# Kernel tuning notes

Measured on AMD Instinct MI355X. Metric: run time of the kernel, lower is better.

## Reference

```python
import jax, jax.numpy as jnp
import numpy as np

B, T, C = 2, 2048, 1024
N_HEAD, N_GROUP = 16, 4
N_KV = N_HEAD // N_GROUP          # 4
HEAD_DIM = C // N_HEAD            # 64
ROPE_BASE = 10000.0
INIT_STD = 0.02


def setup_inputs() -> dict:
    key = jax.random.key(0)
    ks = jax.random.split(key, 5)
    kvC = N_KV * HEAD_DIM
    return {
        "x": jax.random.normal(ks[0], (B, T, C), jnp.float32),
        "w_q": jax.random.normal(ks[1], (C, C), jnp.float32) * INIT_STD,
        "b_q": jnp.zeros((C,), jnp.float32),
        "w_k": jax.random.normal(ks[2], (C, kvC), jnp.float32) * INIT_STD,
        "b_k": jnp.zeros((kvC,), jnp.float32),
        "w_v": jax.random.normal(ks[3], (C, kvC), jnp.float32) * INIT_STD,
        "b_v": jnp.zeros((kvC,), jnp.float32),
        "w_o": jax.random.normal(ks[4], (C, C), jnp.float32) * INIT_STD,
        "b_o": jnp.zeros((C,), jnp.float32),
    }


def reference(x, w_q, b_q, w_k, b_k, w_v, b_v, w_o, b_o):
    Bx, Tx, Cx = x.shape
    # projections (torch Linear math with weights stored as [in, out])
    q = (x @ w_q + b_q).reshape(Bx, Tx, N_HEAD, HEAD_DIM).transpose(0, 2, 1, 3)  # [B,H,T,hd]
    k = (x @ w_k + b_k).reshape(Bx, Tx, N_KV, HEAD_DIM).transpose(0, 2, 1, 3)    # [B,KV,T,hd]
    v = (x @ w_v + b_v).reshape(Bx, Tx, N_KV, HEAD_DIM).transpose(0, 2, 1, 3)

    # RoPE with INTERLEAVED pair convention: pairs are (dim 2i, dim 2i+1)
    inv_freq = 1.0 / (ROPE_BASE ** (jnp.arange(0, HEAD_DIM, 2, dtype=jnp.float32) / HEAD_DIM))
    freqs = jnp.arange(Tx, dtype=jnp.float32)[:, None] * inv_freq[None, :]       # [T, hd/2]
    cos, sin = jnp.cos(freqs), jnp.sin(freqs)

    def rope(t):
        tp = t.reshape(*t.shape[:-1], HEAD_DIM // 2, 2)
        e, o = tp[..., 0], tp[..., 1]          # even/odd lanes, [B,h,T,hd/2]
        er = e * cos - o * sin
        orr = e * sin + o * cos
        return jnp.stack([er, orr], axis=-1).reshape(t.shape)

    q, k = rope(q), rope(k)

    # GQA: duplicate each KV head n_group times (consecutively, like repeat_interleave)
    k = jnp.repeat(k, N_GROUP, axis=1)   # [B,H,T,hd]
    v = jnp.repeat(v, N_GROUP, axis=1)

    attn = jnp.einsum('bhqd,bhkd->bhqk', q, k) / np.sqrt(HEAD_DIM).astype(np.float32)
    causal = jnp.tril(jnp.ones((Tx, Tx), bool))
    attn = jnp.where(causal, attn, -jnp.inf)
    attn = jax.nn.softmax(attn, axis=-1)

    out = jnp.einsum('bhqk,bhkd->bhqd', attn, v)            # [B,H,T,hd]
    out = out.transpose(0, 2, 1, 3).reshape(Bx, Tx, Cx)
    return out @ w_o + b_o
```

## Files before the change

kernel.cpp:

```cpp
#include <hip/hip_runtime.h>
#include <hip/hip_bf16.h>

typedef __hip_bfloat16 bf16;
typedef __attribute__((ext_vector_type(8))) short short8_t;
typedef __attribute__((ext_vector_type(4))) short short4_t;
typedef __attribute__((ext_vector_type(4))) float f32x4;

#define B_SZ   2
#define T_SEQ  2048
#define C_DIM  1024
#define NH     16
#define NKV    4
#define HD     64
#define QKVW   1536
#define MTOK   (B_SZ * T_SEQ)

#define LOG2_BASE_OVER_32 0.4152410118609203f
#define Q_SCALE 0.1803368801111204f

__device__ __forceinline__ short f2bs(float f) {
    unsigned u = __float_as_uint(f);
    u += 0x7FFFu + ((u >> 16) & 1u);
    return (short)(u >> 16);
}
__device__ __forceinline__ short f2bs_trunc(float f) {
    return (short)(__float_as_uint(f) >> 16);
}
__device__ __forceinline__ float bs2f(short s) {
    unsigned u = ((unsigned)(unsigned short)s) << 16;
    return __uint_as_float(u);
}
__device__ __forceinline__ float dpp_xor1(float x) {
    return __int_as_float(
        __builtin_amdgcn_update_dpp(0, __float_as_int(x), 0xB1, 0xF, 0xF, true));
}

__device__ __forceinline__ void transpose_tile(
    const float* __restrict__ W, short* __restrict__ Wt,
    int K, int N, int n0, int k0, int tid)
{
    __shared__ float tile[32][33];
    int tx = tid & 31, ty = tid >> 5;
    #pragma unroll
    for (int i = 0; i < 4; ++i)
        tile[ty + 8 * i][tx] = W[(size_t)(k0 + ty + 8 * i) * N + n0 + tx];
    __syncthreads();
    #pragma unroll
    for (int i = 0; i < 4; ++i)
        Wt[(size_t)(n0 + ty + 8 * i) * K + k0 + tx] = f2bs(tile[tx][ty + 8 * i]);
}

__global__ __launch_bounds__(256) void prep_kernel(
    const float* __restrict__ x,
    const float* __restrict__ w_q, const float* __restrict__ w_k,
    const float* __restrict__ w_v, const float* __restrict__ w_o,
    const float* __restrict__ b_q, const float* __restrict__ b_k,
    const float* __restrict__ b_v,
    short* __restrict__ Xb, short* __restrict__ Wqkv, short* __restrict__ Wto,
    float* __restrict__ Bqkv, float2* __restrict__ Tab)
{
    int blk = blockIdx.x, tid = threadIdx.x;
    if (blk < 4096) {
        int i = blk * 1024 + tid * 4;
        float4 v = *(const float4*)(x + i);
        short4_t o;
        o[0] = f2bs(v.x); o[1] = f2bs(v.y); o[2] = f2bs(v.z); o[3] = f2bs(v.w);
        *(short4_t*)(Xb + i) = o;
    } else if (blk < 5120) {
        int l = blk - 4096;
        transpose_tile(w_q, Wqkv, C_DIM, C_DIM, (l & 31) * 32, (l >> 5) * 32, tid);
    } else if (blk < 5376) {
        int l = blk - 5120;
        transpose_tile(w_k, Wqkv + (size_t)1024 * C_DIM, C_DIM, 256,
                       (l & 7) * 32, (l >> 3) * 32, tid);
    } else if (blk < 5632) {
        int l = blk - 5376;
        transpose_tile(w_v, Wqkv + (size_t)1280 * C_DIM, C_DIM, 256,
                       (l & 7) * 32, (l >> 3) * 32, tid);
    } else if (blk < 6656) {
        int l = blk - 5632;
        transpose_tile(w_o, Wto, C_DIM, C_DIM, (l & 31) * 32, (l >> 5) * 32, tid);
    } else if (blk < 6662) {
        int i = (blk - 6656) * 256 + tid;
        float v;
        if (i < 1024)      v = b_q[i];
        else if (i < 1280) v = b_k[i - 1024];
        else               v = b_v[i - 1280];
        Bqkv[i] = v;
    } else {
        int idx = (blk - 6662) * 256 + tid;
        int t = idx >> 5, i = idx & 31;
        float ang = (float)t * exp2f(-(float)i * LOG2_BASE_OVER_32);
        Tab[idx] = make_float2(cosf(ang), sinf(ang));
    }
}

__global__ __launch_bounds__(256) void gemm_qkv(
    const short* __restrict__ A, const short* __restrict__ Bt,
    const float* __restrict__ bias, const float2* __restrict__ Tab,
    short* __restrict__ QKVb, short* __restrict__ Vt)
{
    __shared__ __align__(16) short smem[20480];
    typedef short lds_tile_t[128][40];
    lds_tile_t* sA = (lds_tile_t*)smem;
    lds_tile_t* sB = (lds_tile_t*)(smem + 10240);

    const int K = C_DIM, N = QKVW;
    int m0 = blockIdx.y * 128;
    int n0 = blockIdx.x * 128;
    int tid  = threadIdx.x;
    int w    = tid >> 6, lane = tid & 63;
    int quad = lane >> 4, l16 = lane & 15;
    int wm = w & 1, wn = w >> 1;

    f32x4 acc[4][4] = {};

    short8_t ra[2], rb[2];
    #pragma unroll
    for (int it = 0; it < 2; ++it) {
        int slot = tid + 256 * it, row = slot >> 2, g = (slot & 3) * 8;
        ra[it] = *(const short8_t*)(A  + (size_t)(m0 + row) * K + g);
        rb[it] = *(const short8_t*)(Bt + (size_t)(n0 + row) * K + g);
    }

    int buf = 0;
    for (int k0 = 0; k0 < K; k0 += 32, buf ^= 1) {
        #pragma unroll
        for (int it = 0; it < 2; ++it) {
            int slot = tid + 256 * it, row = slot >> 2, g = (slot & 3) * 8;
            *(short8_t*)&sA[buf][row][g] = ra[it];
            *(short8_t*)&sB[buf][row][g] = rb[it];
        }
        if (k0 + 32 < K) {
            #pragma unroll
            for (int it = 0; it < 2; ++it) {
                int slot = tid + 256 * it, row = slot >> 2, g = (slot & 3) * 8;
                ra[it] = *(const short8_t*)(A  + (size_t)(m0 + row) * K + k0 + 32 + g);
                rb[it] = *(const short8_t*)(Bt + (size_t)(n0 + row) * K + k0 + 32 + g);
            }
        }
        __syncthreads();

        short8_t af[4], bfr[4];
        #pragma unroll
        for (int mt = 0; mt < 4; ++mt)
            af[mt] = *(const short8_t*)&sA[buf][wm * 64 + mt * 16 + l16][quad * 8];
        #pragma unroll
        for (int nt = 0; nt < 4; ++nt)
            bfr[nt] = *(const short8_t*)&sB[buf][wn * 64 + nt * 16 + l16][quad * 8];
        #pragma unroll
        for (int mt = 0; mt < 4; ++mt)
            #pragma unroll
            for (int nt = 0; nt < 4; ++nt)
                acc[mt][nt] = __builtin_amdgcn_mfma_f32_16x16x32_bf16(
                    af[mt], bfr[nt], acc[mt][nt], 0, 0, 0);
    }

    if (n0 < 1280) {
        float scale = (n0 < 1024) ? Q_SCALE : 1.0f;
        float sgn   = (l16 & 1) ? 1.0f : -1.0f;
        #pragma unroll
        for (int nt = 0; nt < 4; ++nt) {
            int col = n0 + wn * 64 + nt * 16 + l16;
            int ip  = (col & 63) >> 1;
            float bv = bias[col];
            #pragma unroll
            for (int mt = 0; mt < 4; ++mt) {
                #pragma unroll
                for (int r = 0; r < 4; ++r) {
                    int row = m0 + wm * 64 + mt * 16 + quad * 4 + r;
                    float v = acc[mt][nt][r] + bv;
                    float po = dpp_xor1(v);
                    float2 cs = Tab[(row & (T_SEQ - 1)) * 32 + ip];
                    float res = (v * cs.x + sgn * po * cs.y) * scale;
                    QKVb[(size_t)row * QKVW + col] = f2bs(res);
                }
            }
        }
    } else {
        __syncthreads();
        short (*sT)[136] = (short(*)[136])smem;
        #pragma unroll
        for (int nt = 0; nt < 4; ++nt) {
            int col_l = wn * 64 + nt * 16 + l16;
            float bv = bias[n0 + col_l];
            #pragma unroll
            for (int mt = 0; mt < 4; ++mt)
                #pragma unroll
                for (int r = 0; r < 4; ++r)
                    sT[col_l][wm * 64 + mt * 16 + quad * 4 + r] =
                        f2bs(acc[mt][nt][r] + bv);
        }
        __syncthreads();
        int d0 = n0 - 1280;
        #pragma unroll
        for (int it = 0; it < 8; ++it) {
            int slot = tid + 256 * it;
            int dl = slot >> 4, seg = (slot & 15) * 8;
            *(short8_t*)(Vt + (size_t)(d0 + dl) * MTOK + m0 + seg) =
                *(const short8_t*)&sT[dl][seg];
        }
    }
}

__global__ __launch_bounds__(256) void gemm_mfma_o(
    const short* __restrict__ A, const short* __restrict__ Bt,
    const float* __restrict__ bias, float* __restrict__ C,
    int M, int N, int K)
{
    __shared__ __align__(16) short sA[2][128][40];
    __shared__ __align__(16) short sB[2][128][40];

    int m0 = blockIdx.y * 128;
    int n0 = blockIdx.x * 128;
    int tid  = threadIdx.x;
    int w    = tid >> 6, lane = tid & 63;
    int quad = lane >> 4, l16 = lane & 15;
    int wm = w & 1, wn = w >> 1;

    f32x4 acc[4][4] = {};

    short8_t ra[2], rb[2];
    #pragma unroll
    for (int it = 0; it < 2; ++it) {
        int slot = tid + 256 * it, row = slot >> 2, g = (slot & 3) * 8;
        ra[it] = *(const short8_t*)(A  + (size_t)(m0 + row) * K + g);
        rb[it] = *(const short8_t*)(Bt + (size_t)(n0 + row) * K + g);
    }

    int buf = 0;
    for (int k0 = 0; k0 < K; k0 += 32, buf ^= 1) {
        #pragma unroll
        for (int it = 0; it < 2; ++it) {
            int slot = tid + 256 * it, row = slot >> 2, g = (slot & 3) * 8;
            *(short8_t*)&sA[buf][row][g] = ra[it];
            *(short8_t*)&sB[buf][row][g] = rb[it];
        }
        if (k0 + 32 < K) {
            #pragma unroll
            for (int it = 0; it < 2; ++it) {
                int slot = tid + 256 * it, row = slot >> 2, g = (slot & 3) * 8;
                ra[it] = *(const short8_t*)(A  + (size_t)(m0 + row) * K + k0 + 32 + g);
                rb[it] = *(const short8_t*)(Bt + (size_t)(n0 + row) * K + k0 + 32 + g);
            }
        }
        __syncthreads();

        short8_t af[4], bfr[4];
        #pragma unroll
        for (int mt = 0; mt < 4; ++mt)
            af[mt] = *(const short8_t*)&sA[buf][wm * 64 + mt * 16 + l16][quad * 8];
        #pragma unroll
        for (int nt = 0; nt < 4; ++nt)
            bfr[nt] = *(const short8_t*)&sB[buf][wn * 64 + nt * 16 + l16][quad * 8];
        #pragma unroll
        for (int mt = 0; mt < 4; ++mt)
            #pragma unroll
            for (int nt = 0; nt < 4; ++nt)
                acc[mt][nt] = __builtin_amdgcn_mfma_f32_16x16x32_bf16(
                    af[mt], bfr[nt], acc[mt][nt], 0, 0, 0);
    }

    #pragma unroll
    for (int mt = 0; mt < 4; ++mt) {
        #pragma unroll
        for (int nt = 0; nt < 4; ++nt) {
            int col = n0 + wn * 64 + nt * 16 + l16;
            float bv = bias[col];
            #pragma unroll
            for (int r = 0; r < 4; ++r) {
                int row = m0 + wm * 64 + mt * 16 + quad * 4 + r;
                C[(size_t)row * N + col] = acc[mt][nt][r] + bv;
            }
        }
    }
}

__global__ __launch_bounds__(256) void attn_mfma7(
    const short* __restrict__ QKV, const short* __restrict__ Vt,
    short* __restrict__ O)
{
    __shared__ __align__(16) short sK [128][72];
    __shared__ __align__(16) short sVt[64][136];
    __shared__ __align__(16) short sP [4][16][136];

    const int tid  = threadIdx.x;
    const int w    = tid >> 6;
    const int lane = tid & 63;
    const int quad = lane >> 4;
    const int l16  = lane & 15;

    int blk = blockIdx.x;
    int grp = blk & 7;
    int tq  = 127 - (blk >> 3);
    int kvh = grp & 3;
    int b   = grp >> 2;
    int h   = kvh * 4 + w;
    int ct  = (tq * 16 + 15) >> 7;
    int tg  = tq * 16 + l16;

    const short* qptr = QKV + ((size_t)(b * T_SEQ + tq * 16 + l16)) * QKVW + h * HD;
    short8_t qf0 = *(const short8_t*)(qptr + quad * 8);
    short8_t qf1 = *(const short8_t*)(qptr + quad * 8 + 32);

    const short* kbase  = QKV + (size_t)b * T_SEQ * QKVW + 1024 + kvh * HD;
    const short* vtbase = Vt + (size_t)(kvh * HD) * MTOK + b * T_SEQ;

    float m_l = -INFINITY, l_l = 0.f;
    f32x4 oacc[4];
    #pragma unroll
    for (int dt = 0; dt < 4; ++dt) oacc[dt] = (f32x4){0.f, 0.f, 0.f, 0.f};

    short8_t kr[4], vr[4];
    #pragma unroll
    for (int it = 0; it < 4; ++it) {
        int slot = tid + 256 * it;
        kr[it] = *(const short8_t*)(kbase + (size_t)(slot >> 3) * QKVW + (slot & 7) * 8);
        vr[it] = *(const short8_t*)(vtbase + (size_t)(slot >> 4) * MTOK + (slot & 15) * 8);
    }

    for (int c = 0; c <= ct; ++c) {
        __syncthreads();
        #pragma unroll
        for (int it = 0; it < 4; ++it) {
            int slot = tid + 256 * it;
            *(short8_t*)&sK [slot >> 3][(slot & 7) * 8]  = kr[it];
            *(short8_t*)&sVt[slot >> 4][(slot & 15) * 8] = vr[it];
        }
        __syncthreads();
        if (c < ct) {
            int jn = (c + 1) * 128;
            #pragma unroll
            for (int it = 0; it < 4; ++it) {
                int slot = tid + 256 * it;
                kr[it] = *(const short8_t*)(kbase + (size_t)(jn + (slot >> 3)) * QKVW + (slot & 7) * 8);
                vr[it] = *(const short8_t*)(vtbase + (size_t)(slot >> 4) * MTOK + jn + (slot & 15) * 8);
            }
        }

        f32x4 sacc[8];
        #pragma unroll
        for (int kt = 0; kt < 8; ++kt) {
            f32x4 z = {0.f, 0.f, 0.f, 0.f};
            short8_t kf0 = *(const short8_t*)&sK[l16 + 16 * kt][quad * 8];
            short8_t kf1 = *(const short8_t*)&sK[l16 + 16 * kt][quad * 8 + 32];
            z = __builtin_amdgcn_mfma_f32_16x16x32_bf16(kf0, qf0, z, 0, 0, 0);
            z = __builtin_amdgcn_mfma_f32_16x16x32_bf16(kf1, qf1, z, 0, 0, 0);
            sacc[kt] = z;
        }

        if (c == ct) {
            int j0 = c * 128;
            #pragma unroll
            for (int kt = 0; kt < 8; ++kt)
                #pragma unroll
                for (int r = 0; r < 4; ++r)
                    if (j0 + 16 * kt + quad * 4 + r > tg) sacc[kt][r] = -INFINITY;
        }

        float vmax = sacc[0][0];
        #pragma unroll
        for (int kt = 0; kt < 8; ++kt)
            #pragma unroll
            for (int r = 0; r < 4; ++r) vmax = fmaxf(vmax, sacc[kt][r]);
        vmax = fmaxf(vmax, __shfl_xor(vmax, 16));
        vmax = fmaxf(vmax, __shfl_xor(vmax, 32));
        float mnew = fmaxf(m_l, vmax);
        float al = exp2f(m_l - mnew);
        m_l = mnew;

        float psum = 0.f;
        #pragma unroll
        for (int kt = 0; kt < 8; ++kt) {
            short4_t pk;
            #pragma unroll
            for (int r = 0; r < 4; ++r) {
                float p = exp2f(sacc[kt][r] - mnew);
                psum += p;
                pk[r] = f2bs_trunc(p);
            }
            *(short4_t*)&sP[w][l16][16 * kt + 4 * quad] = pk;
        }
        psum += __shfl_xor(psum, 16);
        psum += __shfl_xor(psum, 32);
        l_l = l_l * al + psum;

        if (__any(al < 1.f)) {
            #pragma unroll
            for (int r = 0; r < 4; ++r) {
                float alr = __shfl(al, quad * 4 + r);
                #pragma unroll
                for (int dt = 0; dt < 4; ++dt) oacc[dt][r] *= alr;
            }
        }

        short8_t pf[4];
        #pragma unroll
        for (int g = 0; g < 4; ++g)
            pf[g] = *(const short8_t*)&sP[w][l16][32 * g + quad * 8];
        #pragma unroll
        for (int dt = 0; dt < 4; ++dt) {
            #pragma unroll
            for (int g = 0; g < 4; ++g) {
                short8_t vf = *(const short8_t*)&sVt[16 * dt + l16][32 * g + quad * 8];
                oacc[dt] = __builtin_amdgcn_mfma_f32_16x16x32_bf16(pf[g], vf, oacc[dt], 0, 0, 0);
            }
        }
    }

    #pragma unroll
    for (int r = 0; r < 4; ++r) {
        int m = quad * 4 + r;
        float lr = __shfl(l_l, quad * 4 + r);
        float inv = __builtin_amdgcn_rcpf(lr);
        #pragma unroll
        for (int dt = 0; dt < 4; ++dt)
            O[((size_t)b * T_SEQ + tq * 16 + m) * C_DIM + h * HD + 16 * dt + l16] =
                f2bs(oacc[dt][r] * inv);
    }
}

extern "C" void kernel_launch(void* const* d_in, const int* in_sizes, int n_in,
                              void* d_out, int out_size, void* d_ws, size_t ws_size,
                              hipStream_t stream)
{
    const float* x   = (const float*)d_in[0];
    const float* w_q = (const float*)d_in[1];
    const float* b_q = (const float*)d_in[2];
    const float* w_k = (const float*)d_in[3];
    const float* b_k = (const float*)d_in[4];
    const float* w_v = (const float*)d_in[5];
    const float* b_v = (const float*)d_in[6];
    const float* w_o = (const float*)d_in[7];
    const float* b_o = (const float*)d_in[8];
    float* out = (float*)d_out;

    char* ws = (char*)d_ws;
    short*  Xb   = (short*) (ws);
    short*  Ab   = (short*) (ws + ((size_t)8  << 20));
    short*  QKVb = (short*) (ws + ((size_t)16 << 20));
    short*  Wqkv = (short*) (ws + ((size_t)28 << 20));
    short*  Wto  = (short*) (ws + ((size_t)31 << 20));
    float*  Bqkv = (float*) (ws + ((size_t)33 << 20));
    float2* Tab  = (float2*)(ws + ((size_t)33 << 20) + 8192);
    short*  Vt   = (short*) (ws + ((size_t)34 << 20));

    const int M = MTOK;

    prep_kernel<<<6918, 256, 0, stream>>>(
        x, w_q, w_k, w_v, w_o, b_q, b_k, b_v, Xb, Wqkv, Wto, Bqkv, Tab);

    gemm_qkv<<<dim3(QKVW / 128, M / 128), 256, 0, stream>>>(
        Xb, Wqkv, Bqkv, Tab, QKVb, Vt);

    attn_mfma7<<<B_SZ * NKV * 128, 256, 0, stream>>>(QKVb, Vt, Ab);

    gemm_mfma_o<<<dim3(C_DIM / 128, M / 128), 256, 0, stream>>>(
        Ab, Wto, b_o, out, M, C_DIM, C_DIM);
}
```

Baseline: 183.9 us.

## Split attention KV range across two waves per head with LDS merge

Rewrites the attention kernel so each 128-thread block handles one head and 32 query rows. The two waves split the key chunks between them, alternating 64-key chunks, and their partial softmax states are merged through LDS at the end. K and V fragments are now loaded straight from global memory into registers instead of being staged through shared LDS tiles, which removes the per-chunk barriers. The cost is that the K/V sharing across the four GQA heads in a block is lost, so more global/L2 traffic goes to K/V, in exchange for more blocks and independent waves.

Result: slower. 198.0 us (+7.7%).

```diff
diff --git a/kernel.cpp b/kernel.cpp
--- a/kernel.cpp
+++ b/kernel.cpp
@@ -105,7 +105,7 @@
     lds_tile_t* sA = (lds_tile_t*)smem;
     lds_tile_t* sB = (lds_tile_t*)(smem + 10240);
 
-    const int K = C_DIM, N = QKVW;
+    const int K = C_DIM;
     int m0 = blockIdx.y * 128;
     int n0 = blockIdx.x * 128;
     int tid  = threadIdx.x;
@@ -276,13 +276,13 @@
     }
 }
 
-__global__ __launch_bounds__(256) void attn_mfma7(
+__global__ __launch_bounds__(128) void attn_mfma8(
     const short* __restrict__ QKV, const short* __restrict__ Vt,
     short* __restrict__ O)
 {
-    __shared__ __align__(16) short sK [128][72];
-    __shared__ __align__(16) short sVt[64][136];
-    __shared__ __align__(16) short sP [4][16][136];
+    __shared__ __align__(16) short sP[2][2][16][72];
+    __shared__ __align__(16) float mO[2][64][20];
+    __shared__ float msh[2][16], lsh[2][16];
 
     const int tid  = threadIdx.x;
     const int w    = tid >> 6;
@@ -291,132 +291,209 @@
     const int l16  = lane & 15;
 
     int blk = blockIdx.x;
-    int grp = blk & 7;
-    int tq  = 127 - (blk >> 3);
-    int kvh = grp & 3;
-    int b   = grp >> 2;
-    int h   = kvh * 4 + w;
-    int ct  = (tq * 16 + 15) >> 7;
-    int tg  = tq * 16 + l16;
-
-    const short* qptr = QKV + ((size_t)(b * T_SEQ + tq * 16 + l16)) * QKVW + h * HD;
-    short8_t qf0 = *(const short8_t*)(qptr + quad * 8);
-    short8_t qf1 = *(const short8_t*)(qptr + quad * 8 + 32);
-
-    const short* kbase  = QKV + (size_t)b * T_SEQ * QKVW + 1024 + kvh * HD;
-    const short* vtbase = Vt + (size_t)(kvh * HD) * MTOK + b * T_SEQ;
-
-    float m_l = -INFINITY, l_l = 0.f;
-    f32x4 oacc[4];
+    int u   = 63 - (blk >> 5);
+    int bh  = blk & 31;
+    int b   = bh >> 4;
+    int h   = bh & 15;
+    int kvh = h >> 2;
+    int ct  = u >> 1;
+
+    int tgA = u * 32 + l16;
+    int tgB = tgA + 16;
+
+    const short* qptrA = QKV + ((size_t)(b * T_SEQ) + tgA) * QKVW + h * HD;
+    short8_t qA0 = *(const short8_t*)(qptrA + quad * 8);
+    short8_t qA1 = *(const short8_t*)(qptrA + quad * 8 + 32);
+    const short* qptrB = qptrA + (size_t)16 * QKVW;
+    short8_t qB0 = *(const short8_t*)(qptrB + quad * 8);
+    short8_t qB1 = *(const short8_t*)(qptrB + quad * 8 + 32);
+
+    const short* kbase = QKV + (size_t)b * T_SEQ * QKVW + 1024 + kvh * HD;
+    const short* vtb   = Vt + (size_t)(kvh * HD) * MTOK + b * T_SEQ;
+
+    float mA = -INFINITY, lA = 0.f, mB = -INFINITY, lB = 0.f;
+    f32x4 oA[4], oB[4];
     #pragma unroll
-    for (int dt = 0; dt < 4; ++dt) oacc[dt] = (f32x4){0.f, 0.f, 0.f, 0.f};
-
-    short8_t kr[4], vr[4];
-    #pragma unroll
-    for (int it = 0; it < 4; ++it) {
-        int slot = tid + 256 * it;
-        kr[it] = *(const short8_t*)(kbase + (size_t)(slot >> 3) * QKVW + (slot & 7) * 8);
-        vr[it] = *(const short8_t*)(vtbase + (size_t)(slot >> 4) * MTOK + (slot & 15) * 8);
-    }
-
-    for (int c = 0; c <= ct; ++c) {
-        __syncthreads();
-        #pragma unroll
-        for (int it = 0; it < 4; ++it) {
-            int slot = tid + 256 * it;
-            *(short8_t*)&sK [slot >> 3][(slot & 7) * 8]  = kr[it];
-            *(short8_t*)&sVt[slot >> 4][(slot & 15) * 8] = vr[it];
-        }
-        __syncthreads();
-        if (c < ct) {
-            int jn = (c + 1) * 128;
-            #pragma unroll
-            for (int it = 0; it < 4; ++it) {
-                int slot = tid + 256 * it;
-                kr[it] = *(const short8_t*)(kbase + (size_t)(jn + (slot >> 3)) * QKVW + (slot & 7) * 8);
-                vr[it] = *(const short8_t*)(vtbase + (size_t)(slot >> 4) * MTOK + jn + (slot & 15) * 8);
-            }
-        }
-
-        f32x4 sacc[8];
-        #pragma unroll
-        for (int kt = 0; kt < 8; ++kt) {
+    for (int dt = 0; dt < 4; ++dt) {
+        oA[dt] = (f32x4){0.f, 0.f, 0.f, 0.f};
+        oB[dt] = (f32x4){0.f, 0.f, 0.f, 0.f};
+    }
+
+    for (int c = w; c <= ct; c += 2) {
+        int j0 = c * 64;
+
+        short8_t kf[4][2];
+        #pragma unroll
+        for (int kt = 0; kt < 4; ++kt) {
+            const short* kp = kbase + (size_t)(j0 + 16 * kt + l16) * QKVW + quad * 8;
+            kf[kt][0] = *(const short8_t*)(kp);
+            kf[kt][1] = *(const short8_t*)(kp + 32);
+        }
+
+        f32x4 sA4[4], sB4[4];
+        #pragma unroll
+        for (int kt = 0; kt < 4; ++kt) {
             f32x4 z = {0.f, 0.f, 0.f, 0.f};
-            short8_t kf0 = *(const short8_t*)&sK[l16 + 16 * kt][quad * 8];
-            short8_t kf1 = *(const short8_t*)&sK[l16 + 16 * kt][quad * 8 + 32];
-            z = __builtin_amdgcn_mfma_f32_16x16x32_bf16(kf0, qf0, z, 0, 0, 0);
-            z = __builtin_amdgcn_mfma_f32_16x16x32_bf16(kf1, qf1, z, 0, 0, 0);
-            sacc[kt] = z;
+            z = __builtin_amdgcn_mfma_f32_16x16x32_bf16(kf[kt][0], qA0, z, 0, 0, 0);
+            z = __builtin_amdgcn_mfma_f32_16x16x32_bf16(kf[kt][1], qA1, z, 0, 0, 0);
+            sA4[kt] = z;
+            f32x4 y = {0.f, 0.f, 0.f, 0.f};
+            y = __builtin_amdgcn_mfma_f32_16x16x32_bf16(kf[kt][0], qB0, y, 0, 0, 0);
+            y = __builtin_amdgcn_mfma_f32_16x16x32_bf16(kf[kt][1], qB1, y, 0, 0, 0);
+            sB4[kt] = y;
+        }
+
+        short8_t vf[4][2];
+        #pragma unroll
+        for (int dt = 0; dt < 4; ++dt) {
+            const short* vp = vtb + (size_t)(16 * dt + l16) * MTOK + j0 + quad * 8;
+            vf[dt][0] = *(const short8_t*)(vp);
+            vf[dt][1] = *(const short8_t*)(vp + 32);
         }
 
         if (c == ct) {
-            int j0 = c * 128;
-            #pragma unroll
-            for (int kt = 0; kt < 8; ++kt)
-                #pragma unroll
-                for (int r = 0; r < 4; ++r)
-                    if (j0 + 16 * kt + quad * 4 + r > tg) sacc[kt][r] = -INFINITY;
-        }
-
-        float vmax = sacc[0][0];
-        #pragma unroll
-        for (int kt = 0; kt < 8; ++kt)
-            #pragma unroll
-            for (int r = 0; r < 4; ++r) vmax = fmaxf(vmax, sacc[kt][r]);
-        vmax = fmaxf(vmax, __shfl_xor(vmax, 16));
-        vmax = fmaxf(vmax, __shfl_xor(vmax, 32));
-        float mnew = fmaxf(m_l, vmax);
-        float al = exp2f(m_l - mnew);
-        m_l = mnew;
-
-        float psum = 0.f;
-        #pragma unroll
-        for (int kt = 0; kt < 8; ++kt) {
-            short4_t pk;
+            #pragma unroll
+            for (int kt = 0; kt < 4; ++kt)
+                #pragma unroll
+                for (int r = 0; r < 4; ++r) {
+                    int key = j0 + 16 * kt + quad * 4 + r;
+                    if (key > tgA) sA4[kt][r] = -INFINITY;
+                    if (key > tgB) sB4[kt][r] = -INFINITY;
+                }
+        }
+
+        float alA, alB;
+        {
+            float vmax = sA4[0][0];
+            #pragma unroll
+            for (int kt = 0; kt < 4; ++kt)
+                #pragma unroll
+                for (int r = 0; r < 4; ++r) vmax = fmaxf(vmax, sA4[kt][r]);
+            vmax = fmaxf(vmax, __shfl_xor(vmax, 16));
+            vmax = fmaxf(vmax, __shfl_xor(vmax, 32));
+            float mnew = fmaxf(mA, vmax);
+            alA = exp2f(mA - mnew);
+            mA = mnew;
+            float psum = 0.f;
+            #pragma unroll
+            for (int kt = 0; kt < 4; ++kt) {
+                short4_t pk;
+                #pragma unroll
+                for (int r = 0; r < 4; ++r) {
+                    float p = exp2f(sA4[kt][r] - mnew);
+                    psum += p;
+                    pk[r] = f2bs_trunc(p);
+                }
+                *(short4_t*)&sP[w][0][l16][16 * kt + 4 * quad] = pk;
+            }
+            psum += __shfl_xor(psum, 16);
+            psum += __shfl_xor(psum, 32);
+            lA = lA * alA + psum;
+        }
+        {
+            float vmax = sB4[0][0];
+            #pragma unroll
+            for (int kt = 0; kt < 4; ++kt)
+                #pragma unroll
+                for (int r = 0; r < 4; ++r) vmax = fmaxf(vmax, sB4[kt][r]);
+            vmax = fmaxf(vmax, __shfl_xor(vmax, 16));
+            vmax = fmaxf(vmax, __shfl_xor(vmax, 32));
+            float mnew = fmaxf(mB, vmax);
+            alB = exp2f(mB - mnew);
+            mB = mnew;
+            float psum = 0.f;
+            #pragma unroll
+            for (int kt = 0; kt < 4; ++kt) {
+                short4_t pk;
+                #pragma unroll
+                for (int r = 0; r < 4; ++r) {
+                    float p = exp2f(sB4[kt][r] - mnew);
+                    psum += p;
+                    pk[r] = f2bs_trunc(p);
+                }
+                *(short4_t*)&sP[w][1][l16][16 * kt + 4 * quad] = pk;
+            }
+            psum += __shfl_xor(psum, 16);
+            psum += __shfl_xor(psum, 32);
+            lB = lB * alB + psum;
+        }
+
+        if (__any(alA < 1.f)) {
             #pragma unroll
             for (int r = 0; r < 4; ++r) {
-                float p = exp2f(sacc[kt][r] - mnew);
-                psum += p;
-                pk[r] = f2bs_trunc(p);
-            }
-            *(short4_t*)&sP[w][l16][16 * kt + 4 * quad] = pk;
-        }
-        psum += __shfl_xor(psum, 16);
-        psum += __shfl_xor(psum, 32);
-        l_l = l_l * al + psum;
-
-        if (__any(al < 1.f)) {
+                float ar = __shfl(alA, quad * 4 + r);
+                #pragma unroll
+                for (int dt = 0; dt < 4; ++dt) oA[dt][r] *= ar;
+            }
+        }
+        if (__any(alB < 1.f)) {
             #pragma unroll
             for (int r = 0; r < 4; ++r) {
-                float alr = __shfl(al, quad * 4 + r);
-                #pragma unroll
-                for (int dt = 0; dt < 4; ++dt) oacc[dt][r] *= alr;
-            }
-        }
-
-        short8_t pf[4];
-        #pragma unroll
-        for (int g = 0; g < 4; ++g)
-            pf[g] = *(const short8_t*)&sP[w][l16][32 * g + quad * 8];
+                float ar = __shfl(alB, quad * 4 + r);
+                #pragma unroll
+                for (int dt = 0; dt < 4; ++dt) oB[dt][r] *= ar;
+            }
+        }
+
+        short8_t pfA0 = *(const short8_t*)&sP[w][0][l16][quad * 8];
+        short8_t pfA1 = *(const short8_t*)&sP[w][0][l16][quad * 8 + 32];
         #pragma unroll
         for (int dt = 0; dt < 4; ++dt) {
-            #pragma unroll
-            for (int g = 0; g < 4; ++g) {
-                short8_t vf = *(const short8_t*)&sVt[16 * dt + l16][32 * g + quad * 8];
-                oacc[dt] = __builtin_amdgcn_mfma_f32_16x16x32_bf16(pf[g], vf, oacc[dt], 0, 0, 0);
-            }
-        }
-    }
-
-    #pragma unroll
-    for (int r = 0; r < 4; ++r) {
-        int m = quad * 4 + r;
-        float lr = __shfl(l_l, quad * 4 + r);
-        float inv = __builtin_amdgcn_rcpf(lr);
-        #pragma unroll
-        for (int dt = 0; dt < 4; ++dt)
-            O[((size_t)b * T_SEQ + tq * 16 + m) * C_DIM + h * HD + 16 * dt + l16] =
-                f2bs(oacc[dt][r] * inv);
+            oA[dt] = __builtin_amdgcn_mfma_f32_16x16x32_bf16(pfA0, vf[dt][0], oA[dt], 0, 0, 0);
+            oA[dt] = __builtin_amdgcn_mfma_f32_16x16x32_bf16(pfA1, vf[dt][1], oA[dt], 0, 0, 0);
+        }
+        short8_t pfB0 = *(const short8_t*)&sP[w][1][l16][quad * 8];
+        short8_t pfB1 = *(const short8_t*)&sP[w][1][l16][quad * 8 + 32];
+        #pragma unroll
+        for (int dt = 0; dt < 4; ++dt) {
+            oB[dt] = __builtin_amdgcn_mfma_f32_16x16x32_bf16(pfB0, vf[dt][0], oB[dt], 0, 0, 0);
+            oB[dt] = __builtin_amdgcn_mfma_f32_16x16x32_bf16(pfB1, vf[dt][1], oB[dt], 0, 0, 0);
+        }
+    }
+
+    if (w == 1) {
+        #pragma unroll
+        for (int dt = 0; dt < 4; ++dt) {
+            *(f32x4*)&mO[0][16 * dt + l16][quad * 4] = oA[dt];
+            *(f32x4*)&mO[1][16 * dt + l16][quad * 4] = oB[dt];
+        }
+        if (quad == 0) {
+            msh[0][l16] = mA; lsh[0][l16] = lA;
+            msh[1][l16] = mB; lsh[1][l16] = lB;
+        }
+    }
+    __syncthreads();
+    if (w == 0) {
+        #pragma unroll
+        for (int tile = 0; tile < 2; ++tile) {
+            float m0 = (tile == 0) ? mA : mB;
+            float l0 = (tile == 0) ? lA : lB;
+            float m1 = msh[tile][l16];
+            float l1 = lsh[tile][l16];
+            float mstar = fmaxf(m0, m1);
+            float a0 = exp2f(m0 - mstar);
+            float a1 = exp2f(m1 - mstar);
+            float inv = __builtin_amdgcn_rcpf(l0 * a0 + l1 * a1);
+            float a0r[4], a1r[4], invr[4];
+            #pragma unroll
+            for (int r = 0; r < 4; ++r) {
+                a0r[r]  = __shfl(a0,  quad * 4 + r);
+                a1r[r]  = __shfl(a1,  quad * 4 + r);
+                invr[r] = __shfl(inv, quad * 4 + r);
+            }
+            #pragma unroll
+            for (int dt = 0; dt < 4; ++dt) {
+                f32x4 ov = *(const f32x4*)&mO[tile][16 * dt + l16][quad * 4];
+                f32x4 oc = (tile == 0) ? oA[dt] : oB[dt];
+                #pragma unroll
+                for (int r = 0; r < 4; ++r) {
+                    float res = (oc[r] * a0r[r] + ov[r] * a1r[r]) * invr[r];
+                    int row = u * 32 + tile * 16 + quad * 4 + r;
+                    O[((size_t)b * T_SEQ + row) * C_DIM + h * HD + 16 * dt + l16] =
+                        f2bs(res);
+                }
+            }
+        }
     }
 }
 
@@ -453,7 +530,7 @@
     gemm_qkv<<<dim3(QKVW / 128, M / 128), 256, 0, stream>>>(
         Xb, Wqkv, Bqkv, Tab, QKVb, Vt);
 
-    attn_mfma7<<<B_SZ * NKV * 128, 256, 0, stream>>>(QKVb, Vt, Ab);
+    attn_mfma8<<<2048, 128, 0, stream>>>(QKVb, Vt, Ab);
 
     gemm_mfma_o<<<dim3(C_DIM / 128, M / 128), 256, 0, stream>>>(
         Ab, Wto, b_o, out, M, C_DIM, C_DIM);
```
